# Kernel tuning notes

Measured on AMD Instinct MI355X. Metric: run time of the kernel, lower is better.

## Reference

```python
import jax, jax.numpy as jnp
import numpy as np

B, N, C = 32, 1024, 768
H = 12
HD = C // H            # 64
M = 2 * HD             # rand_feat_dim = head_dim * rand_feat_dim_ratio(2) = 128
LAM = 0.1
NUM_STEP = 8
EPS = 1e-12


def setup_inputs() -> dict:
    key = jax.random.key(0)
    ks = jax.random.split(key, 4)
    x = jax.random.normal(ks[0], (B, N, C), dtype=jnp.float32)
    qkv_w = jax.random.normal(ks[1], (2 * C, C), dtype=jnp.float32) * 0.02
    proj_w = jax.random.normal(ks[2], (C, C), dtype=jnp.float32) * 0.02
    proj_b = jnp.zeros((C,), dtype=jnp.float32)
    rand_matrix = jax.random.normal(ks[3], (H, HD, M), dtype=jnp.float32)
    learned_k = jnp.eye(M, dtype=jnp.float32)
    learned_lam = jnp.ones((1,), dtype=jnp.float32)
    learned_L = jnp.ones((1,), dtype=jnp.float32)
    return {"x": x, "qkv_w": qkv_w, "proj_w": proj_w, "proj_b": proj_b,
            "rand_matrix": rand_matrix, "learned_k": learned_k,
            "learned_lam": learned_lam, "learned_L": learned_L}


def _soft(z, thresh):
    # sign(z) * GELU(|z| - thresh), exact (erf) GELU as in torch nn.GELU()
    return jnp.sign(z) * jax.nn.gelu(jnp.abs(z) - thresh, approximate=False)


def reference(x, qkv_w, proj_w, proj_b, rand_matrix, learned_k, learned_lam, learned_L):
    scale = HD ** -0.5
    qkv = (x @ qkv_w.T).reshape(B, N, 2, H, HD).transpose(2, 0, 3, 1, 4)  # [2,B,H,N,HD]
    q, v = qkv[0], qkv[1]
    q = q * (scale ** 0.5)
    # performer-style positive random features: exp(x @ proj - ||x||^2/2)/sqrt(m)
    qf = jnp.exp(jnp.einsum('bhnd,hdm->bhnm', q, rand_matrix)
                 - jnp.sum(q * q, axis=-1, keepdims=True) / 2) / (M ** 0.5)
    # F.normalize(p=2, dim=-2): normalize each feature column over tokens
    qf = qf / jnp.maximum(jnp.linalg.norm(qf, axis=-2, keepdims=True), EPS)
    kk = jnp.einsum('bhnm,bhnp->bhmp', qf, qf)        # [B,H,M,M]
    inp = jnp.einsum('bhnm,bhnd->bhmd', qf, v)        # [B,H,M,HD]
    # ISTA-like sparse reconstruction
    L = jax.lax.stop_gradient(jnp.max(jnp.sum(jnp.abs(kk), axis=-1), axis=-1))[..., None, None] + 1.0
    lam_learned = learned_lam * LAM                    # broadcastable scalar
    Ll = L / learned_L                                 # [B,H,1,1]
    kk_l = jnp.einsum('mp,bhpq,qr->bhmr', learned_k, kk, learned_k)
    xs = _soft(inp, lam_learned)
    for _ in range(NUM_STEP):
        xs = xs - (jnp.einsum('bhmp,bhpd->bhmd', kk_l, xs) - inp) / Ll
        xs = _soft(xs, lam_learned / Ll)
    out = jnp.einsum('bhnm,bhmd->bhnd', qf, xs)        # [B,H,N,HD]
    out = out.transpose(0, 2, 1, 3).reshape(B, N, C)
    return out @ proj_w.T + proj_b
```

## Files before the change

kernel.cpp:

```cpp
#include <hip/hip_runtime.h>
#include <math.h>

typedef unsigned short u16;
typedef unsigned int u32;
typedef _Float16 f16;
typedef __attribute__((ext_vector_type(8))) short bf16x8;
typedef __attribute__((ext_vector_type(8))) _Float16 f16x8;
typedef __attribute__((ext_vector_type(4))) float f32x4;

constexpr int Bc = 32, Nc = 1024, Cc = 768, Hc = 12, HDc = 64, Mc = 128;
constexpr int NUM_STEP_C = 8;
constexpr float QSCALE = 0.35355339059327376f;
constexpr float INV_SQRT_M = 0.088388347648318447f;
constexpr float EPSC = 1e-12f;
constexpr int FS = 136;

__device__ __forceinline__ float softf(float z, float thr) {
  float az = fabsf(z) - thr;
  float g = 0.5f * az * (1.0f + erff(az * 0.70710678118654752f));
  return (z > 0.f) ? g : ((z < 0.f) ? -g : 0.f);
}

__device__ __forceinline__ u16 f2bf(float f) {
  u32 u = __float_as_uint(f);
  u += 0x7fffu + ((u >> 16) & 1u);
  return (u16)(u >> 16);
}

__device__ __forceinline__ f32x4 fzero() {
  f32x4 z; z[0] = 0.f; z[1] = 0.f; z[2] = 0.f; z[3] = 0.f; return z;
}

__device__ __forceinline__ f32x4 mfma16(bf16x8 a, bf16x8 b, f32x4 c) {
  return __builtin_amdgcn_mfma_f32_16x16x32_bf16(a, b, c, 0, 0, 0);
}
__device__ __forceinline__ f32x4 mfma16h(f16x8 a, f16x8 b, f32x4 c) {
  return __builtin_amdgcn_mfma_f32_16x16x32_f16(a, b, c, 0, 0, 0);
}

#define SWZ_COL(col, row) ((col) ^ (((row) & 7) << 3))

__device__ __forceinline__ void stage_swz(const u16* __restrict__ g, int ld,
                                          u16* lds, int w, int lane) {
  const int rr = lane >> 3;
  const int cs = ((lane & 7) ^ rr) << 3;
#pragma unroll
  for (int c = 0; c < 4; ++c) {
    const int r0 = w * 32 + c * 8;
    __builtin_amdgcn_global_load_lds(
        (const __attribute__((address_space(1))) void*)(g + (size_t)(r0 + rr) * ld + cs),
        (__attribute__((address_space(3))) void*)(lds + r0 * 64), 16, 0, 0);
  }
}

__global__ __launch_bounds__(256) void prep_kernel(
    const float* __restrict__ x, const float* __restrict__ qw,
    const float* __restrict__ pw, const float* __restrict__ rnd,
    const float* __restrict__ lkf, u16* __restrict__ xbf,
    u16* __restrict__ wbf, u16* __restrict__ pwbf, u16* __restrict__ randt,
    f16* __restrict__ lk16, f16* __restrict__ lkT16) {
  const int NX8 = 3145728, NW8 = 147456, NP8 = 73728, NR = 98304;
  const int NK8 = 2048, NKT = 16384;
  const int total = NX8 + NW8 + NP8 + NR + NK8 + NKT;
  for (int idx = blockIdx.x * 256 + threadIdx.x; idx < total;
       idx += gridDim.x * 256) {
    if (idx < NX8 + NW8 + NP8) {
      const float* src; u16* dst; int k;
      if (idx < NX8) { src = x; dst = xbf; k = idx; }
      else if (idx < NX8 + NW8) { src = qw; dst = wbf; k = idx - NX8; }
      else { src = pw; dst = pwbf; k = idx - NX8 - NW8; }
      float4 a = *(const float4*)(src + (size_t)k * 8);
      float4 b = *(const float4*)(src + (size_t)k * 8 + 4);
      uint4 o;
      o.x = (u32)f2bf(a.x) | ((u32)f2bf(a.y) << 16);
      o.y = (u32)f2bf(a.z) | ((u32)f2bf(a.w) << 16);
      o.z = (u32)f2bf(b.x) | ((u32)f2bf(b.y) << 16);
      o.w = (u32)f2bf(b.z) | ((u32)f2bf(b.w) << 16);
      *(uint4*)(dst + (size_t)k * 8) = o;
    } else if (idx < NX8 + NW8 + NP8 + NR) {
      int k = idx - NX8 - NW8 - NP8;
      int h = k >> 13, rem = k & 8191, m = rem >> 6, d = rem & 63;
      randt[k] = f2bf(rnd[(size_t)h * 8192 + d * 128 + m]);
    } else if (idx < NX8 + NW8 + NP8 + NR + NK8) {
      int k = idx - (NX8 + NW8 + NP8 + NR);
      float4 a = *(const float4*)(lkf + (size_t)k * 8);
      float4 b = *(const float4*)(lkf + (size_t)k * 8 + 4);
      union { f16 h[8]; uint4 u; } z;
      z.h[0] = (f16)a.x; z.h[1] = (f16)a.y; z.h[2] = (f16)a.z; z.h[3] = (f16)a.w;
      z.h[4] = (f16)b.x; z.h[5] = (f16)b.y; z.h[6] = (f16)b.z; z.h[7] = (f16)b.w;
      *(uint4*)(lk16 + (size_t)k * 8) = z.u;
    } else {
      int k = idx - (NX8 + NW8 + NP8 + NR + NK8);
      int c = k >> 7, p = k & 127;
      lkT16[k] = (f16)lkf[p * 128 + c];
    }
  }
}

__global__ __launch_bounds__(256) void qkv_qf_kernel(
    const u16* __restrict__ xbf, const u16* __restrict__ wbf,
    const u16* __restrict__ randt, u16* __restrict__ qft,
    u16* __restrict__ vbt) {
  __shared__ __align__(16) u16 SH[32768];
  const int t = threadIdx.x;
  const int hblk = blockIdx.x;
  const int lin = (hblk & 7) * 384 + (hblk >> 3);
  const int bi = lin / 12, bj = lin % 12;
  const int w = t >> 6, lane = t & 63, ln = lane & 15, kg = lane >> 4;
  const int wr = w >> 1, wc = w & 1;
  f32x4 acc[4][4];
#pragma unroll
  for (int i = 0; i < 4; ++i)
#pragma unroll
    for (int j = 0; j < 4; ++j) acc[i][j] = fzero();
  const u16* Ag = xbf + (size_t)(bi * 128) * Cc;
  const u16* Bg = wbf + (size_t)(bj * 128) * Cc;
  stage_swz(Ag, Cc, SH, w, lane);
  stage_swz(Bg, Cc, SH + 8192, w, lane);
  __syncthreads();
  int cur = 0;
  for (int tt = 0; tt < 12; ++tt) {
    if (tt < 11) {
      stage_swz(Ag + (tt + 1) * 64, Cc, SH + (cur ^ 1) * 16384, w, lane);
      stage_swz(Bg + (tt + 1) * 64, Cc, SH + 8192 + (cur ^ 1) * 16384, w, lane);
    }
    const u16* Als = SH + cur * 16384;
    const u16* Bls = SH + 8192 + cur * 16384;
#pragma unroll
    for (int ks = 0; ks < 2; ++ks) {
      const int cb = ks * 32 + kg * 8;
      bf16x8 af[4], bf[4];
#pragma unroll
      for (int i = 0; i < 4; ++i)
        af[i] = *(const bf16x8*)(Als + (wr * 64 + i * 16 + ln) * 64 +
                                 SWZ_COL(cb, ln));
#pragma unroll
      for (int j = 0; j < 4; ++j)
        bf[j] = *(const bf16x8*)(Bls + (wc * 64 + j * 16 + ln) * 64 +
                                 SWZ_COL(cb, ln));
#pragma unroll
      for (int i = 0; i < 4; ++i)
#pragma unroll
        for (int j = 0; j < 4; ++j) acc[i][j] = mfma16(af[i], bf[j], acc[i][j]);
    }
    __syncthreads();
    cur ^= 1;
  }
  const int b = bi >> 3;
  const int ntile = (bi & 7) * 128;
  if (bj >= 6) {
    const int h = (bj - 6) * 2 + wc;
    u16* vt = vbt + ((size_t)(b * Hc + h) * 64) * 1024;
#pragma unroll
    for (int i = 0; i < 4; ++i)
#pragma unroll
      for (int j = 0; j < 4; ++j) {
        int d = j * 16 + ln;
        int n0 = ntile + wr * 64 + i * 16 + kg * 4;
        uint2 pv;
        pv.x = (u32)f2bf(acc[i][j][0]) | ((u32)f2bf(acc[i][j][1]) << 16);
        pv.y = (u32)f2bf(acc[i][j][2]) | ((u32)f2bf(acc[i][j][3]) << 16);
        *(uint2*)(vt + (size_t)d * 1024 + n0) = pv;
      }
  } else {
#pragma unroll
    for (int i = 0; i < 4; ++i)
#pragma unroll
      for (int j = 0; j < 4; ++j) acc[i][j] *= QSCALE;
    float hn[4][4];
#pragma unroll
    for (int i = 0; i < 4; ++i)
#pragma unroll
      for (int r = 0; r < 4; ++r) {
        float s = acc[i][0][r] * acc[i][0][r] + acc[i][1][r] * acc[i][1][r] +
                  acc[i][2][r] * acc[i][2][r] + acc[i][3][r] * acc[i][3][r];
        s += __shfl_xor(s, 1); s += __shfl_xor(s, 2);
        s += __shfl_xor(s, 4); s += __shfl_xor(s, 8);
        hn[i][r] = 0.5f * s;
      }
    u16* Qls = SH;
#pragma unroll
    for (int i = 0; i < 4; ++i)
#pragma unroll
      for (int j = 0; j < 4; ++j)
#pragma unroll
        for (int r = 0; r < 4; ++r)
          Qls[(size_t)(wc * 128 + wr * 64 + i * 16 + kg * 4 + r) * 72 +
              j * 16 + ln] = f2bf(acc[i][j][r]);
    __syncthreads();
    const int hq = bj * 2 + (w & 1);
    const int r0q = (w >> 1) * 64;
    const u16* rt = randt + (size_t)hq * Mc * HDc;
    u16* qtb = qft + ((size_t)(b * Hc + hq) * Mc) * Nc;
    const u16* qsl = Qls + (size_t)(w & 1) * 128 * 72;
#pragma unroll
    for (int mh = 0; mh < 2; ++mh) {
      f32x4 a2[4][4];
#pragma unroll
      for (int i = 0; i < 4; ++i)
#pragma unroll
        for (int j = 0; j < 4; ++j) a2[i][j] = fzero();
#pragma unroll
      for (int ks = 0; ks < 2; ++ks) {
        bf16x8 af[4], bfr[4];
#pragma unroll
        for (int i = 0; i < 4; ++i)
          af[i] = *(const bf16x8*)(qsl + (size_t)(r0q + i * 16 + ln) * 72 +
                                   ks * 32 + kg * 8);
#pragma unroll
        for (int j = 0; j < 4; ++j)
          bfr[j] = *(const bf16x8*)(rt +
                                    (size_t)(mh * 64 + j * 16 + ln) * 64 +
                                    ks * 32 + kg * 8);
#pragma unroll
        for (int i = 0; i < 4; ++i)
#pragma unroll
          for (int j = 0; j < 4; ++j)
            a2[i][j] = mfma16(af[i], bfr[j], a2[i][j]);
      }
#pragma unroll
      for (int i = 0; i < 4; ++i)
#pragma unroll
        for (int j = 0; j < 4; ++j) {
          const int m = mh * 64 + j * 16 + ln;
          const int n0 = ntile + r0q + i * 16 + kg * 4;
          float e0 = __expf(a2[i][j][0] - hn[i][0]) * INV_SQRT_M;
          float e1 = __expf(a2[i][j][1] - hn[i][1]) * INV_SQRT_M;
          float e2 = __expf(a2[i][j][2] - hn[i][2]) * INV_SQRT_M;
          float e3 = __expf(a2[i][j][3] - hn[i][3]) * INV_SQRT_M;
          uint2 pv;
          pv.x = (u32)f2bf(e0) | ((u32)f2bf(e1) << 16);
          pv.y = (u32)f2bf(e2) | ((u32)f2bf(e3) << 16);
          *(uint2*)(qtb + (size_t)m * Nc + n0) = pv;
        }
    }
  }
}

__global__ __launch_bounds__(384) void kk_inp_kernel(
    const u16* __restrict__ qft, const u16* __restrict__ vbt,
    float* __restrict__ kk, float* __restrict__ inp) {
  __shared__ __align__(16) u16 SH[24576];
  const int t = threadIdx.x, bh = blockIdx.x;
  const int w = t >> 6, lane = t & 63, ln = lane & 15, kg = lane >> 4;
  const int wr = w / 3, wc = w % 3;
  const u16* qg = qft + (size_t)bh * Mc * Nc;
  const u16* vg = vbt + (size_t)bh * 64 * Nc;
  const int rr = lane >> 3;
  const int cs = ((lane & 7) ^ rr) << 3;
  f32x4 acc[4][4];
#pragma unroll
  for (int i = 0; i < 4; ++i)
#pragma unroll
    for (int j = 0; j < 4; ++j) acc[i][j] = fzero();

  auto stage = [&](int kt, int buf) {
    u16* Atl = SH + buf * 12288;
    u16* Vtl = Atl + 8192;
    const int n0 = kt * 64;
#pragma unroll
    for (int q = 0; q < 4; ++q) {
      const int idx = w * 4 + q;
      if (idx < 16) {
        __builtin_amdgcn_global_load_lds(
            (const __attribute__((address_space(1))) void*)(
                qg + (size_t)(idx * 8 + rr) * Nc + n0 + cs),
            (__attribute__((address_space(3))) void*)(Atl + idx * 8 * 64), 16,
            0, 0);
      } else {
        __builtin_amdgcn_global_load_lds(
            (const __attribute__((address_space(1))) void*)(
                vg + (size_t)((idx - 16) * 8 + rr) * Nc + n0 + cs),
            (__attribute__((address_space(3))) void*)(Vtl + (idx - 16) * 8 * 64),
            16, 0, 0);
      }
    }
  };

  stage(0, 0);
  __syncthreads();
  int cur = 0;
  for (int kt = 0; kt < 16; ++kt) {
    if (kt < 15) stage(kt + 1, cur ^ 1);
    const u16* Atl = SH + cur * 12288;
    const u16* Vtl = Atl + 8192;
#pragma unroll
    for (int ks = 0; ks < 2; ++ks) {
      const int cb = ks * 32 + kg * 8;
      bf16x8 af[4], bf[4];
#pragma unroll
      for (int i = 0; i < 4; ++i)
        af[i] = *(const bf16x8*)(Atl + (wr * 64 + i * 16 + ln) * 64 +
                                 SWZ_COL(cb, ln));
      if (wc < 2) {
#pragma unroll
        for (int j = 0; j < 4; ++j)
          bf[j] = *(const bf16x8*)(Atl + (wc * 64 + j * 16 + ln) * 64 +
                                   SWZ_COL(cb, ln));
      } else {
#pragma unroll
        for (int j = 0; j < 4; ++j)
          bf[j] = *(const bf16x8*)(Vtl + (j * 16 + ln) * 64 + SWZ_COL(cb, ln));
      }
#pragma unroll
      for (int i = 0; i < 4; ++i)
#pragma unroll
        for (int j = 0; j < 4; ++j) acc[i][j] = mfma16(af[i], bf[j], acc[i][j]);
    }
    __syncthreads();
    cur ^= 1;
  }
  if (wc < 2) {
    float* og = kk + (size_t)bh * Mc * Mc;
#pragma unroll
    for (int i = 0; i < 4; ++i)
#pragma unroll
      for (int j = 0; j < 4; ++j)
#pragma unroll
        for (int r = 0; r < 4; ++r)
          og[(size_t)(wr * 64 + i * 16 + kg * 4 + r) * Mc + wc * 64 + j * 16 +
             ln] = acc[i][j][r];
  } else {
    float* og = inp + (size_t)bh * Mc * HDc;
#pragma unroll
    for (int i = 0; i < 4; ++i)
#pragma unroll
      for (int j = 0; j < 4; ++j)
#pragma unroll
        for (int r = 0; r < 4; ++r)
          og[(size_t)(wr * 64 + i * 16 + kg * 4 + r) * HDc + j * 16 + ln] =
              acc[i][j][r];
  }
}

__global__ __launch_bounds__(256) void solve_kernel(
    const float* __restrict__ kk, const float* __restrict__ inp,
    const f16* __restrict__ lk16, const f16* __restrict__ lkT16,
    const float* __restrict__ lamp, const float* __restrict__ Lp,
    const u16* __restrict__ qft, u16* __restrict__ attn) {
  __shared__ __align__(16) f16 A1[128 * FS];
  __shared__ __align__(16) f16 B1[128 * FS];
  __shared__ float nrm[128], inr[128];
  __shared__ float rsum2[256];
  __shared__ float Lsh;
  const int t = threadIdx.x, bh = blockIdx.x;
  const int w = t >> 6, lane = t & 63, ln = lane & 15, kq = lane >> 4;
  const float* kkg = kk + (size_t)bh * 16384;
  if (t < 128) {
    float nm = fmaxf(sqrtf(kkg[t * 128 + t]), EPSC);
    nrm[t] = nm;
    inr[t] = 1.0f / nm;
  }
#pragma unroll
  for (int c = 0; c < 8; ++c) {
    int ch = c * 256 + t;
    int r = ch >> 4, q8 = (ch & 15) * 8;
    *(uint4*)&B1[r * FS + q8] = *(const uint4*)&lkT16[r * 128 + q8];
  }
  __syncthreads();
#pragma unroll
  for (int c = 0; c < 16; ++c) {
    int ch = c * 256 + t;
    int m = ch >> 5, p4 = (ch & 31) * 4;
    float4 v = *(const float4*)&kkg[m * 128 + p4];
    float im = inr[m];
    union { f16 h[4]; uint2 u; } z;
    z.h[0] = (f16)(v.x * im * inr[p4]);
    z.h[1] = (f16)(v.y * im * inr[p4 + 1]);
    z.h[2] = (f16)(v.z * im * inr[p4 + 2]);
    z.h[3] = (f16)(v.w * im * inr[p4 + 3]);
    *(uint2*)&A1[m * FS + p4] = z.u;
  }
  __syncthreads();
  {
    const int m = t & 127, hf = (t >> 7) * 64;
    float s = 0.f;
#pragma unroll 8
    for (int p = 0; p < 64; ++p) s += fabsf((float)A1[m * FS + hf + p]);
    rsum2[t] = s;
  }
  f32x4 t1a[2][8];
#pragma unroll
  for (int i = 0; i < 2; ++i)
#pragma unroll
    for (int j = 0; j < 8; ++j) t1a[i][j] = fzero();
  __syncthreads();
  if (t == 0) {
    float mx = 0.f;
    for (int i = 0; i < 128; ++i) mx = fmaxf(mx, rsum2[i] + rsum2[i + 128]);
    Lsh = mx + 1.0f;
  }
#pragma unroll
  for (int ks = 0; ks < 4; ++ks) {
    f16x8 a[2], b[8];
#pragma unroll
    for (int i = 0; i < 2; ++i)
      a[i] = *(const f16x8*)&A1[(w * 32 + i * 16 + ln) * FS + ks * 32 + kq * 8];
#pragma unroll
    for (int j = 0; j < 8; ++j)
      b[j] = *(const f16x8*)&B1[(j * 16 + ln) * FS + ks * 32 + kq * 8];
#pragma unroll
    for (int i = 0; i < 2; ++i)
#pragma unroll
      for (int j = 0; j < 8; ++j) t1a[i][j] = mfma16h(a[i], b[j], t1a[i][j]);
  }
  __syncthreads();
#pragma unroll
  for (int i = 0; i < 2; ++i)
#pragma unroll
    for (int j = 0; j < 8; ++j) {
      const int r = j * 16 + ln, p0 = w * 32 + i * 16 + kq * 4;
      union { f16 h[4]; uint2 u; } z;
      z.h[0] = (f16)t1a[i][j][0]; z.h[1] = (f16)t1a[i][j][1];
      z.h[2] = (f16)t1a[i][j][2]; z.h[3] = (f16)t1a[i][j][3];
      *(uint2*)&A1[r * FS + p0] = z.u;
    }
#pragma unroll
  for (int c = 0; c < 8; ++c) {
    int ch = c * 256 + t;
    int r = ch >> 4, q8 = (ch & 15) * 8;
    *(uint4*)&B1[r * FS + q8] = *(const uint4*)&lk16[r * 128 + q8];
  }
  __syncthreads();
  f32x4 kla[2][8];
#pragma unroll
  for (int i = 0; i < 2; ++i)
#pragma unroll
    for (int j = 0; j < 8; ++j) kla[i][j] = fzero();
#pragma unroll
  for (int ks = 0; ks < 4; ++ks) {
    f16x8 a[2], b[8];
#pragma unroll
    for (int i = 0; i < 2; ++i)
      a[i] = *(const f16x8*)&B1[(w * 32 + i * 16 + ln) * FS + ks * 32 + kq * 8];
#pragma unroll
    for (int j = 0; j < 8; ++j)
      b[j] = *(const f16x8*)&A1[(j * 16 + ln) * FS + ks * 32 + kq * 8];
#pragma unroll
    for (int i = 0; i < 2; ++i)
#pragma unroll
      for (int j = 0; j < 8; ++j) kla[i][j] = mfma16h(a[i], b[j], kla[i][j]);
  }
  __syncthreads();
#pragma unroll
  for (int i = 0; i < 2; ++i)
#pragma unroll
    for (int j = 0; j < 8; ++j)
#pragma unroll
      for (int r = 0; r < 4; ++r)
        B1[(w * 32 + i * 16 + kq * 4 + r) * FS + j * 16 + ln] =
            (f16)kla[i][j][r];
  const float lam = lamp[0] * 0.1f;
  const float Ll = Lsh / Lp[0];
  const float thr = lam / Ll;
  const float invLl = 1.0f / Ll;
  const float* ig = inp + (size_t)bh * 8192;
  float ri[2][4][4], xr[2][4][4];
#pragma unroll
  for (int i = 0; i < 2; ++i)
#pragma unroll
    for (int j = 0; j < 4; ++j)
#pragma unroll
      for (int r = 0; r < 4; ++r) {
        const int m = w * 32 + i * 16 + kq * 4 + r;
        const int d = j * 16 + ln;
        ri[i][j][r] = ig[m * 64 + d] * inr[m];
        xr[i][j][r] = softf(ri[i][j][r], lam);
      }
  __syncthreads();
#pragma unroll
  for (int i = 0; i < 2; ++i)
#pragma unroll
    for (int j = 0; j < 4; ++j) {
      const int d = j * 16 + ln, m0 = w * 32 + i * 16 + kq * 4;
      union { f16 h[4]; uint2 u; } z;
      z.h[0] = (f16)xr[i][j][0]; z.h[1] = (f16)xr[i][j][1];
      z.h[2] = (f16)xr[i][j][2]; z.h[3] = (f16)xr[i][j][3];
      *(uint2*)&A1[d * FS + m0] = z.u;
    }
  __syncthreads();
  for (int s = 0; s < NUM_STEP_C; ++s) {
    f32x4 acc[2][4];
#pragma unroll
    for (int i = 0; i < 2; ++i)
#pragma unroll
      for (int j = 0; j < 4; ++j) acc[i][j] = fzero();
#pragma unroll
    for (int ks = 0; ks < 4; ++ks) {
      f16x8 a[2], b[4];
#pragma unroll
      for (int i = 0; i < 2; ++i)
        a[i] = *(const f16x8*)&B1[(w * 32 + i * 16 + ln) * FS + ks * 32 + kq * 8];
#pragma unroll
      for (int j = 0; j < 4; ++j)
        b[j] = *(const f16x8*)&A1[(j * 16 + ln) * FS + ks * 32 + kq * 8];
#pragma unroll
      for (int i = 0; i < 2; ++i)
#pragma unroll
        for (int j = 0; j < 4; ++j) acc[i][j] = mfma16h(a[i], b[j], acc[i][j]);
    }
#pragma unroll
    for (int i = 0; i < 2; ++i)
#pragma unroll
      for (int j = 0; j < 4; ++j)
#pragma unroll
        for (int r = 0; r < 4; ++r)
          xr[i][j][r] =
              softf(xr[i][j][r] - (acc[i][j][r] - ri[i][j][r]) * invLl, thr);
    __syncthreads();
#pragma unroll
    for (int i = 0; i < 2; ++i)
#pragma unroll
      for (int j = 0; j < 4; ++j) {
        const int d = j * 16 + ln, m0 = w * 32 + i * 16 + kq * 4;
        union { f16 h[4]; uint2 u; } z;
        z.h[0] = (f16)xr[i][j][0]; z.h[1] = (f16)xr[i][j][1];
        z.h[2] = (f16)xr[i][j][2]; z.h[3] = (f16)xr[i][j][3];
        *(uint2*)&A1[d * FS + m0] = z.u;
      }
    __syncthreads();
  }
  u16* A1u = (u16*)A1;
#pragma unroll
  for (int i = 0; i < 2; ++i)
#pragma unroll
    for (int j = 0; j < 4; ++j) {
      const int d = j * 16 + ln, m0 = w * 32 + i * 16 + kq * 4;
      uint2 pv;
      pv.x = (u32)f2bf(xr[i][j][0] * inr[m0]) |
             ((u32)f2bf(xr[i][j][1] * inr[m0 + 1]) << 16);
      pv.y = (u32)f2bf(xr[i][j][2] * inr[m0 + 2]) |
             ((u32)f2bf(xr[i][j][3] * inr[m0 + 3]) << 16);
      *(uint2*)&A1u[d * FS + m0] = pv;
    }
  __syncthreads();
  const u16* qt = qft + (size_t)bh * Mc * Nc;
  const int b = bh / Hc, h = bh % Hc;
  for (int nt = 0; nt < 8; ++nt) {
    f32x4 pacc[2][4];
#pragma unroll
    for (int i = 0; i < 2; ++i)
#pragma unroll
      for (int j = 0; j < 4; ++j) pacc[i][j] = fzero();
#pragma unroll
    for (int ks = 0; ks < 4; ++ks) {
      const int m8 = ks * 32 + kq * 8;
      bf16x8 af[2];
#pragma unroll
      for (int i = 0; i < 2; ++i) {
        const int n = nt * 128 + w * 32 + i * 16 + ln;
        const u16* p = qt + (size_t)m8 * Nc + n;
#pragma unroll
        for (int e = 0; e < 8; ++e) af[i][e] = (short)p[(size_t)e * Nc];
      }
      bf16x8 bf[4];
#pragma unroll
      for (int j = 0; j < 4; ++j)
        bf[j] = *(const bf16x8*)&A1u[(j * 16 + ln) * FS + m8];
#pragma unroll
      for (int i = 0; i < 2; ++i)
#pragma unroll
        for (int j = 0; j < 4; ++j)
          pacc[i][j] = mfma16(af[i], bf[j], pacc[i][j]);
    }
#pragma unroll
    for (int i = 0; i < 2; ++i)
#pragma unroll
      for (int j = 0; j < 4; ++j)
#pragma unroll
        for (int r = 0; r < 4; ++r) {
          int n = nt * 128 + w * 32 + i * 16 + kq * 4 + r;
          attn[((size_t)(b * Nc + n)) * Cc + h * 64 + j * 16 + ln] =
              f2bf(pacc[i][j][r]);
        }
  }
}

__global__ __launch_bounds__(256) void proj_kernel(
    const u16* __restrict__ abf, const u16* __restrict__ pwbf,
    const float* __restrict__ bias, float* __restrict__ out) {
  __shared__ __align__(16) u16 SH[32768];
  const int t = threadIdx.x;
  const int hblk = blockIdx.x;
  const int lin = (hblk & 7) * 192 + (hblk >> 3);
  const int bi = lin / 6, bj = lin % 6;
  const int w = t >> 6, lane = t & 63, ln = lane & 15, kg = lane >> 4;
  const int wr = w >> 1, wc = w & 1;
  f32x4 acc[4][4];
#pragma unroll
  for (int i = 0; i < 4; ++i)
#pragma unroll
    for (int j = 0; j < 4; ++j) acc[i][j] = fzero();
  const u16* Ag = abf + (size_t)(bi * 128) * Cc;
  const u16* Bg = pwbf + (size_t)(bj * 128) * Cc;
  stage_swz(Ag, Cc, SH, w, lane);
  stage_swz(Bg, Cc, SH + 8192, w, lane);
  __syncthreads();
  int cur = 0;
  for (int tt = 0; tt < 12; ++tt) {
    if (tt < 11) {
      stage_swz(Ag + (tt + 1) * 64, Cc, SH + (cur ^ 1) * 16384, w, lane);
      stage_swz(Bg + (tt + 1) * 64, Cc, SH + 8192 + (cur ^ 1) * 16384, w, lane);
    }
    const u16* Als = SH + cur * 16384;
    const u16* Bls = SH + 8192 + cur * 16384;
#pragma unroll
    for (int ks = 0; ks < 2; ++ks) {
      const int cb = ks * 32 + kg * 8;
      bf16x8 af[4], bf[4];
#pragma unroll
      for (int i = 0; i < 4; ++i)
        af[i] = *(const bf16x8*)(Als + (wr * 64 + i * 16 + ln) * 64 +
                                 SWZ_COL(cb, ln));
#pragma unroll
      for (int j = 0; j < 4; ++j)
        bf[j] = *(const bf16x8*)(Bls + (wc * 64 + j * 16 + ln) * 64 +
                                 SWZ_COL(cb, ln));
#pragma unroll
      for (int i = 0; i < 4; ++i)
#pragma unroll
        for (int j = 0; j < 4; ++j) acc[i][j] = mfma16(af[i], bf[j], acc[i][j]);
    }
    __syncthreads();
    cur ^= 1;
  }
#pragma unroll
  for (int j = 0; j < 4; ++j) {
    const int gc = bj * 128 + wc * 64 + j * 16 + ln;
    const float bv = bias[gc];
#pragma unroll
    for (int i = 0; i < 4; ++i) {
      const int gr = bi * 128 + wr * 64 + i * 16 + kg * 4;
#pragma unroll
      for (int r = 0; r < 4; ++r)
        out[(size_t)(gr + r) * Cc + gc] = acc[i][j][r] + bv;
    }
  }
}

extern "C" void kernel_launch(void* const* d_in, const int* in_sizes, int n_in,
                              void* d_out, int out_size, void* d_ws,
                              size_t ws_size, hipStream_t stream) {
  const float* x = (const float*)d_in[0];
  const float* qkv_w = (const float*)d_in[1];
  const float* proj_w = (const float*)d_in[2];
  const float* proj_b = (const float*)d_in[3];
  const float* rand_matrix = (const float*)d_in[4];
  const float* learned_k = (const float*)d_in[5];
  const float* learned_lam = (const float*)d_in[6];
  const float* learned_L = (const float*)d_in[7];
  float* out = (float*)d_out;

  const size_t SX = 25165824;
  const size_t SQF = 50331648;
  const size_t SVT = 25165824;
  const size_t SW = 1179648;
  const size_t SPW = 589824;
  const size_t SRT = 98304;
  const size_t SLK = 16384;
  const size_t U16TOT = SX + SQF + SVT + SW + SPW + SRT + 2 * SLK;
  const size_t SKK = 6291456, SIN = 3145728;
  const size_t need = U16TOT * 2 + (SKK + SIN) * 4;
  if (ws_size < need) return;

  u16* xbf = (u16*)d_ws;
  u16* qft = xbf + SX;
  u16* vbt = qft + SQF;
  u16* wbf = vbt + SVT;
  u16* pwbf = wbf + SW;
  u16* randt = pwbf + SPW;
  f16* lk16 = (f16*)(randt + SRT);
  f16* lkT16 = lk16 + SLK;
  float* kkf = (float*)(lkT16 + SLK);
  float* inpf = kkf + SKK;
  u16* attnbf = xbf;

  prep_kernel<<<2048, 256, 0, stream>>>(x, qkv_w, proj_w, rand_matrix,
                                        learned_k, xbf, wbf, pwbf, randt,
                                        lk16, lkT16);
  qkv_qf_kernel<<<3072, 256, 0, stream>>>(xbf, wbf, randt, qft, vbt);
  kk_inp_kernel<<<Bc * Hc, 384, 0, stream>>>(qft, vbt, kkf, inpf);
  solve_kernel<<<Bc * Hc, 256, 0, stream>>>(kkf, inpf, lk16, lkT16,
                                            learned_lam, learned_L, qft,
                                            attnbf);
  proj_kernel<<<1536, 256, 0, stream>>>(attnbf, pwbf, proj_b, out);
}
```

Baseline: 380.7 us.

## Stage transposed V/Q-feature stores and final-pass qf reads through swizzled LDS

```diff
diff --git a/kernel.cpp b/kernel.cpp
--- a/kernel.cpp
+++ b/kernel.cpp
@@ -149,19 +149,31 @@
   const int b = bi >> 3;
   const int ntile = (bi & 7) * 128;
   if (bj >= 6) {
-    const int h = (bj - 6) * 2 + wc;
-    u16* vt = vbt + ((size_t)(b * Hc + h) * 64) * 1024;
+    u16* Vb = SH;
 #pragma unroll
     for (int i = 0; i < 4; ++i)
 #pragma unroll
       for (int j = 0; j < 4; ++j) {
-        int d = j * 16 + ln;
-        int n0 = ntile + wr * 64 + i * 16 + kg * 4;
+        const int d = j * 16 + ln;
+        const int nloc = wr * 64 + i * 16 + kg * 4;
         uint2 pv;
         pv.x = (u32)f2bf(acc[i][j][0]) | ((u32)f2bf(acc[i][j][1]) << 16);
         pv.y = (u32)f2bf(acc[i][j][2]) | ((u32)f2bf(acc[i][j][3]) << 16);
-        *(uint2*)(vt + (size_t)d * 1024 + n0) = pv;
-      }
+        *(uint2*)(Vb + wc * 8192 + d * 128 + (nloc ^ ((d & 7) << 3))) = pv;
+      }
+    __syncthreads();
+#pragma unroll
+    for (int c = 0; c < 8; ++c) {
+      const int chunk = t + c * 256;
+      const int li = chunk * 8;
+      const int hh = li >> 13;
+      const int rem = li & 8191;
+      const int d = rem >> 7, c8 = rem & 127;
+      uint4 v = *(const uint4*)(Vb + hh * 8192 + d * 128 +
+                                (c8 ^ ((d & 7) << 3)));
+      const int h = (bj - 6) * 2 + hh;
+      *(uint4*)(vbt + ((size_t)(b * Hc + h) * 64 + d) * 1024 + ntile + c8) = v;
+    }
   } else {
 #pragma unroll
     for (int i = 0; i < 4; ++i)
@@ -188,11 +200,10 @@
           Qls[(size_t)(wc * 128 + wr * 64 + i * 16 + kg * 4 + r) * 72 +
               j * 16 + ln] = f2bf(acc[i][j][r]);
     __syncthreads();
-    const int hq = bj * 2 + (w & 1);
-    const int r0q = (w >> 1) * 64;
-    const u16* rt = randt + (size_t)hq * Mc * HDc;
-    u16* qtb = qft + ((size_t)(b * Hc + hq) * Mc) * Nc;
-    const u16* qsl = Qls + (size_t)(w & 1) * 128 * 72;
+    const int r0q = wr * 64;
+    const u16* rt = randt + (size_t)(bj * 2 + wc) * Mc * HDc;
+    const u16* qsl = Qls + (size_t)wc * 128 * 72;
+    u16* Qb = SH + 18432;
 #pragma unroll
     for (int mh = 0; mh < 2; ++mh) {
       f32x4 a2[4][4];
@@ -219,20 +230,41 @@
             a2[i][j] = mfma16(af[i], bfr[j], a2[i][j]);
       }
 #pragma unroll
-      for (int i = 0; i < 4; ++i)
-#pragma unroll
-        for (int j = 0; j < 4; ++j) {
-          const int m = mh * 64 + j * 16 + ln;
-          const int n0 = ntile + r0q + i * 16 + kg * 4;
-          float e0 = __expf(a2[i][j][0] - hn[i][0]) * INV_SQRT_M;
-          float e1 = __expf(a2[i][j][1] - hn[i][1]) * INV_SQRT_M;
-          float e2 = __expf(a2[i][j][2] - hn[i][2]) * INV_SQRT_M;
-          float e3 = __expf(a2[i][j][3] - hn[i][3]) * INV_SQRT_M;
-          uint2 pv;
-          pv.x = (u32)f2bf(e0) | ((u32)f2bf(e1) << 16);
-          pv.y = (u32)f2bf(e2) | ((u32)f2bf(e3) << 16);
-          *(uint2*)(qtb + (size_t)m * Nc + n0) = pv;
+      for (int p = 0; p < 2; ++p) {
+        __syncthreads();
+        if (wr == p) {
+#pragma unroll
+          for (int i = 0; i < 4; ++i)
+#pragma unroll
+            for (int j = 0; j < 4; ++j) {
+              const int mloc = j * 16 + ln;
+              const int n64 = i * 16 + kg * 4;
+              float e0 = __expf(a2[i][j][0] - hn[i][0]) * INV_SQRT_M;
+              float e1 = __expf(a2[i][j][1] - hn[i][1]) * INV_SQRT_M;
+              float e2 = __expf(a2[i][j][2] - hn[i][2]) * INV_SQRT_M;
+              float e3 = __expf(a2[i][j][3] - hn[i][3]) * INV_SQRT_M;
+              uint2 pv;
+              pv.x = (u32)f2bf(e0) | ((u32)f2bf(e1) << 16);
+              pv.y = (u32)f2bf(e2) | ((u32)f2bf(e3) << 16);
+              *(uint2*)(Qb + wc * 4096 + mloc * 64 +
+                        (n64 ^ ((mloc & 7) << 3))) = pv;
+            }
         }
+        __syncthreads();
+#pragma unroll
+        for (int c = 0; c < 4; ++c) {
+          const int chunk = t + c * 256;
+          const int li = chunk * 8;
+          const int hh = li >> 12;
+          const int rem = li & 4095;
+          const int mloc = rem >> 6, c8 = rem & 63;
+          uint4 v = *(const uint4*)(Qb + hh * 4096 + mloc * 64 +
+                                    (c8 ^ ((mloc & 7) << 3)));
+          u16* qtb = qft + ((size_t)(b * Hc + bj * 2 + hh) * Mc + mh * 64 +
+                            mloc) * Nc;
+          *(uint4*)(qtb + ntile + p * 64 + c8) = v;
+        }
+      }
     }
   }
 }
@@ -533,10 +565,22 @@
              ((u32)f2bf(xr[i][j][3] * inr[m0 + 3]) << 16);
       *(uint2*)&A1u[d * FS + m0] = pv;
     }
-  __syncthreads();
+  u16* QS = (u16*)B1;
   const u16* qt = qft + (size_t)bh * Mc * Nc;
   const int b = bh / Hc, h = bh % Hc;
   for (int nt = 0; nt < 8; ++nt) {
+    __syncthreads();
+#pragma unroll
+    for (int q = 0; q < 8; ++q) {
+      const int m0 = w * 32 + q * 4;
+      const int mrow = m0 + (lane >> 4);
+      const int sp = ((mrow >> 3) & 7) << 3;
+      __builtin_amdgcn_global_load_lds(
+          (const __attribute__((address_space(1))) void*)(
+              qt + (size_t)mrow * Nc + nt * 128 + (((lane & 15) * 8) ^ sp)),
+          (__attribute__((address_space(3))) void*)(QS + m0 * 128), 16, 0, 0);
+    }
+    __syncthreads();
     f32x4 pacc[2][4];
 #pragma unroll
     for (int i = 0; i < 2; ++i)
@@ -545,13 +589,15 @@
 #pragma unroll
     for (int ks = 0; ks < 4; ++ks) {
       const int m8 = ks * 32 + kq * 8;
+      const int sp8 = ((m8 >> 3) & 7) << 3;
       bf16x8 af[2];
 #pragma unroll
       for (int i = 0; i < 2; ++i) {
-        const int n = nt * 128 + w * 32 + i * 16 + ln;
-        const u16* p = qt + (size_t)m8 * Nc + n;
-#pragma unroll
-        for (int e = 0; e < 8; ++e) af[i][e] = (short)p[(size_t)e * Nc];
+        const int nl = w * 32 + i * 16 + ln;
+        const int cidx = nl ^ sp8;
+#pragma unroll
+        for (int e = 0; e < 8; ++e)
+          af[i][e] = (short)QS[(m8 + e) * 128 + cidx];
       }
       bf16x8 bf[4];
 #pragma unroll
```

Result: slower. 394.5 us (+3.6%).

## Split kk/inp reduction over tokens into two blocks per head

Applied to the files above, without the earlier changes.

```diff
diff --git a/kernel.cpp b/kernel.cpp
--- a/kernel.cpp
+++ b/kernel.cpp
@@ -239,15 +239,18 @@
 
 __global__ __launch_bounds__(384) void kk_inp_kernel(
     const u16* __restrict__ qft, const u16* __restrict__ vbt,
-    float* __restrict__ kk, float* __restrict__ inp) {
+    float* __restrict__ kk0, float* __restrict__ kk1,
+    float* __restrict__ inp0, float* __restrict__ inp1) {
   __shared__ __align__(16) u16 SH[24576];
-  const int t = threadIdx.x, bh = blockIdx.x;
+  const int t = threadIdx.x;
+  const int bh = blockIdx.x >> 1, half = blockIdx.x & 1;
   const int w = t >> 6, lane = t & 63, ln = lane & 15, kg = lane >> 4;
   const int wr = w / 3, wc = w % 3;
   const u16* qg = qft + (size_t)bh * Mc * Nc;
   const u16* vg = vbt + (size_t)bh * 64 * Nc;
   const int rr = lane >> 3;
   const int cs = ((lane & 7) ^ rr) << 3;
+  const int kt0 = half * 8;
   f32x4 acc[4][4];
 #pragma unroll
   for (int i = 0; i < 4; ++i)
@@ -277,11 +280,11 @@
     }
   };
 
-  stage(0, 0);
+  stage(kt0, 0);
   __syncthreads();
   int cur = 0;
-  for (int kt = 0; kt < 16; ++kt) {
-    if (kt < 15) stage(kt + 1, cur ^ 1);
+  for (int kt = 0; kt < 8; ++kt) {
+    if (kt < 7) stage(kt0 + kt + 1, cur ^ 1);
     const u16* Atl = SH + cur * 12288;
     const u16* Vtl = Atl + 8192;
 #pragma unroll
@@ -311,7 +314,7 @@
     cur ^= 1;
   }
   if (wc < 2) {
-    float* og = kk + (size_t)bh * Mc * Mc;
+    float* og = (half ? kk1 : kk0) + (size_t)bh * Mc * Mc;
 #pragma unroll
     for (int i = 0; i < 4; ++i)
 #pragma unroll
@@ -321,7 +324,7 @@
           og[(size_t)(wr * 64 + i * 16 + kg * 4 + r) * Mc + wc * 64 + j * 16 +
              ln] = acc[i][j][r];
   } else {
-    float* og = inp + (size_t)bh * Mc * HDc;
+    float* og = (half ? inp1 : inp0) + (size_t)bh * Mc * HDc;
 #pragma unroll
     for (int i = 0; i < 4; ++i)
 #pragma unroll
@@ -334,7 +337,8 @@
 }
 
 __global__ __launch_bounds__(256) void solve_kernel(
-    const float* __restrict__ kk, const float* __restrict__ inp,
+    const float* __restrict__ kk0, const float* __restrict__ kk1,
+    const float* __restrict__ inp0, const float* __restrict__ inp1,
     const f16* __restrict__ lk16, const f16* __restrict__ lkT16,
     const float* __restrict__ lamp, const float* __restrict__ Lp,
     const u16* __restrict__ qft, u16* __restrict__ attn) {
@@ -345,9 +349,10 @@
   __shared__ float Lsh;
   const int t = threadIdx.x, bh = blockIdx.x;
   const int w = t >> 6, lane = t & 63, ln = lane & 15, kq = lane >> 4;
-  const float* kkg = kk + (size_t)bh * 16384;
+  const float* kkg = kk0 + (size_t)bh * 16384;
+  const float* kkg1 = kk1 + (size_t)bh * 16384;
   if (t < 128) {
-    float nm = fmaxf(sqrtf(kkg[t * 128 + t]), EPSC);
+    float nm = fmaxf(sqrtf(kkg[t * 128 + t] + kkg1[t * 128 + t]), EPSC);
     nrm[t] = nm;
     inr[t] = 1.0f / nm;
   }
@@ -363,12 +368,13 @@
     int ch = c * 256 + t;
     int m = ch >> 5, p4 = (ch & 31) * 4;
     float4 v = *(const float4*)&kkg[m * 128 + p4];
+    float4 v1 = *(const float4*)&kkg1[m * 128 + p4];
     float im = inr[m];
     union { f16 h[4]; uint2 u; } z;
-    z.h[0] = (f16)(v.x * im * inr[p4]);
-    z.h[1] = (f16)(v.y * im * inr[p4 + 1]);
-    z.h[2] = (f16)(v.z * im * inr[p4 + 2]);
-    z.h[3] = (f16)(v.w * im * inr[p4 + 3]);
+    z.h[0] = (f16)((v.x + v1.x) * im * inr[p4]);
+    z.h[1] = (f16)((v.y + v1.y) * im * inr[p4 + 1]);
+    z.h[2] = (f16)((v.z + v1.z) * im * inr[p4 + 2]);
+    z.h[3] = (f16)((v.w + v1.w) * im * inr[p4 + 3]);
     *(uint2*)&A1[m * FS + p4] = z.u;
   }
   __syncthreads();
@@ -454,7 +460,8 @@
   const float Ll = Lsh / Lp[0];
   const float thr = lam / Ll;
   const float invLl = 1.0f / Ll;
-  const float* ig = inp + (size_t)bh * 8192;
+  const float* ig = inp0 + (size_t)bh * 8192;
+  const float* ig1 = inp1 + (size_t)bh * 8192;
   float ri[2][4][4], xr[2][4][4];
 #pragma unroll
   for (int i = 0; i < 2; ++i)
@@ -464,7 +471,7 @@
       for (int r = 0; r < 4; ++r) {
         const int m = w * 32 + i * 16 + kq * 4 + r;
         const int d = j * 16 + ln;
-        ri[i][j][r] = ig[m * 64 + d] * inr[m];
+        ri[i][j][r] = (ig[m * 64 + d] + ig1[m * 64 + d]) * inr[m];
         xr[i][j][r] = softf(ri[i][j][r], lam);
       }
   __syncthreads();
@@ -660,7 +667,7 @@
   const size_t SLK = 16384;
   const size_t U16TOT = SX + SQF + SVT + SW + SPW + SRT + 2 * SLK;
   const size_t SKK = 6291456, SIN = 3145728;
-  const size_t need = U16TOT * 2 + (SKK + SIN) * 4;
+  const size_t need = U16TOT * 2 + (SKK + SIN) * 8;
   if (ws_size < need) return;
 
   u16* xbf = (u16*)d_ws;
@@ -671,17 +678,20 @@
   u16* randt = pwbf + SPW;
   f16* lk16 = (f16*)(randt + SRT);
   f16* lkT16 = lk16 + SLK;
-  float* kkf = (float*)(lkT16 + SLK);
-  float* inpf = kkf + SKK;
+  float* kk0 = (float*)(lkT16 + SLK);
+  float* kk1 = kk0 + SKK;
+  float* inp0 = kk1 + SKK;
+  float* inp1 = inp0 + SIN;
   u16* attnbf = xbf;
 
   prep_kernel<<<2048, 256, 0, stream>>>(x, qkv_w, proj_w, rand_matrix,
                                         learned_k, xbf, wbf, pwbf, randt,
                                         lk16, lkT16);
   qkv_qf_kernel<<<3072, 256, 0, stream>>>(xbf, wbf, randt, qft, vbt);
-  kk_inp_kernel<<<Bc * Hc, 384, 0, stream>>>(qft, vbt, kkf, inpf);
-  solve_kernel<<<Bc * Hc, 256, 0, stream>>>(kkf, inpf, lk16, lkT16,
-                                            learned_lam, learned_L, qft,
-                                            attnbf);
+  kk_inp_kernel<<<2 * Bc * Hc, 384, 0, stream>>>(qft, vbt, kk0, kk1, inp0,
+                                                 inp1);
+  solve_kernel<<<Bc * Hc, 256, 0, stream>>>(kk0, kk1, inp0, inp1, lk16,
+                                            lkT16, learned_lam, learned_L,
+                                            qft, attnbf);
   proj_kernel<<<1536, 256, 0, stream>>>(attnbf, pwbf, proj_b, out);
 }
```

Result: slower. 407.7 us (+7.1%).
